# Kernel tuning notes

Measured on AMD Instinct MI355X. Metric: run time of the kernel, lower is better.

Reference implementation:

```python
import jax, jax.numpy as jnp
import numpy as np

N = 524288      # points per view
S = 256         # superpoint segments
SEG = N // S    # points per segment (2048 >= 30 -> no small segments)
C = 96          # backbone_out_channels
K = 30          # samples per segment (matching_max_pair//S = 32 >= 30 -> capped at 30)
NEG = 30        # negatives sampled per anchor row
T_SUP = 0.5     # SupConLoss temperature
EPS = 1e-7


def setup_inputs() -> dict:
    key = jax.random.key(0)
    ks = jax.random.split(key, 4)
    view1_feat = jax.random.normal(ks[0], (N, C), jnp.float32)
    view2_feat = jax.random.normal(ks[1], (N, C), jnp.float32)
    region = (jnp.arange(N, dtype=jnp.int32) // SEG).astype(jnp.int32)
    # evenly spaced K sample indices inside each contiguous segment
    off = jnp.linspace(0.0, SEG - 1, K).astype(jnp.int32)
    idx_samples = (jnp.arange(S, dtype=jnp.int32)[:, None] * SEG + off[None, :]).reshape(-1)
    bg_mask = (jnp.arange(S) % 4) == 0  # some background superpoints
    gq_w = jax.random.normal(ks[2], (C, C), jnp.float32) * 0.02
    gk_w = jax.random.normal(ks[3], (C, C), jnp.float32) * 0.02
    z = jnp.zeros((C,), jnp.float32)
    o = jnp.ones((C,), jnp.float32)
    return dict(view1_feat=view1_feat, view2_feat=view2_feat,
                gq_w=gq_w, gq_b=z, gq_gamma=o, gq_beta=z,
                gk_w=gk_w, gk_b=z, gk_gamma=o, gk_beta=z,
                view1_region=region, view2_region=region,
                idx_samples=idx_samples, bg_mask=bg_mask)


def _head(x, w, b, gamma, beta):
    # Linear -> BatchNorm1d (batch stats, training mode) -> ReLU
    y = x @ w.T + b
    mu = y.mean(axis=0)
    var = jnp.var(y, axis=0)
    y = (y - mu) * jax.lax.rsqrt(var + 1e-5) * gamma + beta
    return jax.nn.relu(y)


def _segment_mean(x, seg, n):
    s = jax.ops.segment_sum(x, seg, num_segments=n)
    cnt = jax.ops.segment_sum(jnp.ones((x.shape[0], 1), x.dtype), seg, num_segments=n)
    return s / jnp.maximum(cnt, 1.0)


def _l2norm(x):
    return x / (jnp.linalg.norm(x, axis=1, keepdims=True) + EPS)


def _supcon(sim, pos, neg):
    # SupConLoss(temperature=0.5, scale_by_temperature=False, is_positive_in_denom=True)
    logits = sim / T_SUP
    denom_mask = pos | neg
    neg_inf = jnp.finfo(logits.dtype).min
    lse = jax.scipy.special.logsumexp(jnp.where(denom_mask, logits, neg_inf), axis=1)
    log_prob = logits - lse[:, None]
    row = jnp.sum(jnp.where(pos, log_prob, 0.0), axis=1) / jnp.sum(pos, axis=1).astype(logits.dtype)
    return -jnp.mean(row)


def reference(view1_feat, view2_feat, gq_w, gq_b, gq_gamma, gq_beta,
              gk_w, gk_b, gk_gamma, gk_beta,
              view1_region, view2_region, idx_samples, bg_mask):
    Sk = S * K
    rows = jnp.arange(S)[:, None]

    # ---- Lcon: raw-feature superpoint anchors vs sampled points ----
    anchor = _l2norm(_segment_mean(view2_feat, view2_region, S))          # [S, C]
    samples = _l2norm(view1_feat[idx_samples])                            # [S*K, C]
    sim = anchor @ samples.T                                              # [S, S*K]

    col_seg = jnp.arange(Sk) // K
    pos1 = rows == col_seg[None, :]                                       # block-diagonal positives

    # 30 evenly spaced negatives among the Sk-K non-positive columns per row
    M = Sk - K
    p = jnp.linspace(0.0, M - 1, NEG).astype(jnp.int32)                   # [NEG]
    actual = jnp.where(p[None, :] < rows * K, p[None, :], p[None, :] + K) # skip own block
    neg1 = jnp.zeros((S, Sk), bool).at[jnp.broadcast_to(rows, (S, NEG)), actual].set(True)
    Lcon = _supcon(sim, pos1, neg1)

    # ---- Lcon_2: projected (g_q / g_k head) features, top-k positives, background-split negatives ----
    v2g = _head(view2_feat, gq_w, gq_b, gq_gamma, gq_beta)
    v1g = _head(view1_feat, gk_w, gk_b, gk_gamma, gk_beta)
    anchor2 = _l2norm(_segment_mean(v2g, view2_region, S))
    samples2 = _l2norm(v1g[idx_samples])
    sim2 = anchor2 @ samples2.T                                           # [S, S*K]

    _, tk = jax.lax.top_k(sim2, K)
    pos2 = jnp.zeros((S, Sk), bool).at[jnp.broadcast_to(rows, (S, K)), tk].set(True)

    bg_col = jnp.repeat(bg_mask, K)                                       # [S*K]
    neg2 = jnp.where(bg_mask[:, None], ~bg_col[None, :], bg_col[None, :]) & (~pos1)
    Lcon2 = _supcon(sim2, pos2, neg2)

    return Lcon + Lcon2


if __name__ == '__main__':
    out = reference(**setup_inputs())
    print(out)
```

## Files before the change

kernel.cpp:

```cpp
#include <hip/hip_runtime.h>
#include <math.h>

#define SK 7680
#define NPTS 524288

#define WS_GQ_PART  0
#define WS_GK_PART  6144
#define WS_GQ_SCALE 12288
#define WS_GQ_SHIFT 12384
#define WS_GK_SCALE 12480
#define WS_GK_SHIFT 12576
#define WS_SEGX2    21888
#define WS_SEGG2    46464
#define WS_ANCHOR1  71040
#define WS_ANCHOR2  95616
#define WS_SAMPT    120192
#define WS_SAMP2T   857472
#define WS_SROW     1594752
#define WS_ZERO_CNT 71040

typedef __attribute__((ext_vector_type(8))) short bf16x8;
typedef __attribute__((ext_vector_type(4))) float f32x4;

__device__ __forceinline__ bf16x8 pack8(float4 a, float4 b){
  union { unsigned u[4]; bf16x8 v; } r;
  asm("v_cvt_pk_bf16_f32 %0, %1, %2" : "=v"(r.u[0]) : "v"(a.x), "v"(a.y));
  asm("v_cvt_pk_bf16_f32 %0, %1, %2" : "=v"(r.u[1]) : "v"(a.z), "v"(a.w));
  asm("v_cvt_pk_bf16_f32 %0, %1, %2" : "=v"(r.u[2]) : "v"(b.x), "v"(b.y));
  asm("v_cvt_pk_bf16_f32 %0, %1, %2" : "=v"(r.u[3]) : "v"(b.z), "v"(b.w));
  return r.v;
}
__device__ __forceinline__ float4 ld4(const float* p){
  return *reinterpret_cast<const float4*>(p);
}

#define DS_ISSUE(r0,r1,r2,base,o0,o1,o2)                            \
  asm volatile("ds_read_b128 %0, %3 offset:" #o0 "\n\t"             \
               "ds_read_b128 %1, %3 offset:" #o1 "\n\t"             \
               "ds_read_b128 %2, %3 offset:" #o2                    \
               : "=v"(r0), "=v"(r1), "=v"(r2) : "v"(base));
#define DS_WAIT(n)                                                  \
  asm volatile("s_waitcnt lgkmcnt(" #n ")" ::: "memory");           \
  __builtin_amdgcn_sched_barrier(0);

#define MFMA3(acc, wx0, wx1, wx2)                                   \
  acc=__builtin_amdgcn_mfma_f32_16x16x32_bf16(a0,wx0,acc,0,0,0);    \
  acc=__builtin_amdgcn_mfma_f32_16x16x32_bf16(a1,wx1,acc,0,0,0);    \
  acc=__builtin_amdgcn_mfma_f32_16x16x32_bf16(a2,wx2,acc,0,0,0);

__device__ __forceinline__ void stage_wfrag(const float* __restrict__ W, float* wlds, int w, int l){
  if (w < 3){
    const int g = l >> 4, lr = l & 15;
    #pragma unroll
    for (int ot=0; ot<6; ++ot){
      const float* wr = W + (ot*16+lr)*96 + w*32 + g*8;
      bf16x8 f = pack8(ld4(wr), ld4(wr+4));
      *reinterpret_cast<bf16x8*>(wlds + ((w*6+ot)*64 + l)*4) = f;
    }
  }
}

__global__ __launch_bounds__(256) void stats_both(
    const float* __restrict__ V1, const float* __restrict__ V2,
    const float* __restrict__ Wk, const float* __restrict__ Wq,
    float* __restrict__ gpartK, float* __restrict__ gpartQ,
    float* __restrict__ gseg)
{
  __shared__ __align__(16) float wlds[4608];
  __shared__ float red[192];
  __shared__ float rsg[96];
  const int tid = threadIdx.x;
  const int l = tid & 63, w = tid >> 6;
  const int g = l >> 4, lr = l & 15;
  const int bid = blockIdx.x;
  const bool isv2 = (bid & 1);
  const int sub = bid >> 1;
  const float* X = isv2 ? V2 : V1;
  const float* W = isv2 ? Wq : Wk;

  stage_wfrag(W, wlds, w, l);
  if (tid < 192) red[tid]=0.f;
  if (isv2 && tid < 96) rsg[tid]=0.f;
  __syncthreads();

  const unsigned wbase = (unsigned)(uintptr_t)wlds + (unsigned)(l*16);

  float sY[6], sY2[6];
  #pragma unroll
  for (int ot=0; ot<6; ++ot){ sY[ot]=0.f; sY2[ot]=0.f; }
  float rs[24];
  #pragma unroll
  for (int t=0; t<24; ++t) rs[t]=0.f;

  const long base_row = (long)sub*256 + w*16 + lr;
  const float* xr0 = X + base_row*96 + g*8;

  float4 c0=ld4(xr0), c1=ld4(xr0+4), c2=ld4(xr0+32), c3=ld4(xr0+36), c4=ld4(xr0+64), c5=ld4(xr0+68);

#define STATS_OT(ot, wx0, wx1, wx2) {                               \
    f32x4 acc={0.f,0.f,0.f,0.f};                                    \
    MFMA3(acc, wx0, wx1, wx2)                                       \
    sY[ot]+=acc[0]+acc[1]+acc[2]+acc[3];                            \
    sY2[ot]=fmaf(acc[0],acc[0],fmaf(acc[1],acc[1],                  \
            fmaf(acc[2],acc[2],fmaf(acc[3],acc[3],sY2[ot])))); }

  #pragma unroll 1
  for (int it=0; it<4; ++it){
    float4 n0,n1,n2,n3,n4,n5;
    if (it<3){
      const float* xn = xr0 + (it+1)*6144;
      n0=ld4(xn); n1=ld4(xn+4); n2=ld4(xn+32); n3=ld4(xn+36); n4=ld4(xn+64); n5=ld4(xn+68);
    }
    if (isv2){
      rs[0]+=c0.x; rs[1]+=c0.y; rs[2]+=c0.z; rs[3]+=c0.w;
      rs[4]+=c1.x; rs[5]+=c1.y; rs[6]+=c1.z; rs[7]+=c1.w;
      rs[8]+=c2.x; rs[9]+=c2.y; rs[10]+=c2.z; rs[11]+=c2.w;
      rs[12]+=c3.x; rs[13]+=c3.y; rs[14]+=c3.z; rs[15]+=c3.w;
      rs[16]+=c4.x; rs[17]+=c4.y; rs[18]+=c4.z; rs[19]+=c4.w;
      rs[20]+=c5.x; rs[21]+=c5.y; rs[22]+=c5.z; rs[23]+=c5.w;
    }
    bf16x8 a0 = pack8(c0,c1), a1 = pack8(c2,c3), a2 = pack8(c4,c5);
    bf16x8 wA0,wA1,wA2, wB0,wB1,wB2;
    DS_ISSUE(wA0,wA1,wA2, wbase, 0,6144,12288)
    DS_ISSUE(wB0,wB1,wB2, wbase, 1024,7168,13312)
    DS_WAIT(3) STATS_OT(0, wA0,wA1,wA2)
    DS_ISSUE(wA0,wA1,wA2, wbase, 2048,8192,14336)
    DS_WAIT(3) STATS_OT(1, wB0,wB1,wB2)
    DS_ISSUE(wB0,wB1,wB2, wbase, 3072,9216,15360)
    DS_WAIT(3) STATS_OT(2, wA0,wA1,wA2)
    DS_ISSUE(wA0,wA1,wA2, wbase, 4096,10240,16384)
    DS_WAIT(3) STATS_OT(3, wB0,wB1,wB2)
    DS_ISSUE(wB0,wB1,wB2, wbase, 5120,11264,17408)
    DS_WAIT(3) STATS_OT(4, wA0,wA1,wA2)
    DS_WAIT(0) STATS_OT(5, wB0,wB1,wB2)
    if (it<3){ c0=n0; c1=n1; c2=n2; c3=n3; c4=n4; c5=n5; }
  }
#undef STATS_OT

  #pragma unroll
  for (int ot=0; ot<6; ++ot){
    float s = sY[ot], s2 = sY2[ot];
    s  += __shfl_xor(s,16);  s  += __shfl_xor(s,32);
    s2 += __shfl_xor(s2,16); s2 += __shfl_xor(s2,32);
    if (g==0){
      atomicAdd(&red[ot*16+lr], s);
      atomicAdd(&red[96+ot*16+lr], s2);
    }
  }
  if (isv2){
    #pragma unroll
    for (int t=0; t<24; ++t){
      float s = rs[t];
      s += __shfl_xor(s,1); s += __shfl_xor(s,2);
      s += __shfl_xor(s,4); s += __shfl_xor(s,8);
      if (lr==0){
        int kt = t>>3, j = t&7;
        atomicAdd(&rsg[kt*32 + g*8 + j], s);
      }
    }
  }
  __syncthreads();
  if (tid<96){
    float* dst = (isv2 ? gpartQ : gpartK) + (sub & 31)*192;
    atomicAdd(dst+tid,    red[tid]);
    atomicAdd(dst+96+tid, red[96+tid]);
    if (isv2) atomicAdd(gseg + (sub>>3)*96 + tid, rsg[tid]);
  }
}

__global__ __launch_bounds__(256) void head_apply_mfma(
    const float* __restrict__ X, const float* __restrict__ W,
    const float* __restrict__ scale, const float* __restrict__ shift,
    float* __restrict__ gseg)
{
  __shared__ __align__(16) float wlds[4608];
  __shared__ float red[96];
  const int tid = threadIdx.x;
  const int l = tid & 63, w = tid >> 6;
  const int g = l >> 4, lr = l & 15;

  stage_wfrag(W, wlds, w, l);
  if (tid < 96) red[tid]=0.f;
  __syncthreads();

  const unsigned wbase = (unsigned)(uintptr_t)wlds + (unsigned)(l*16);

  float sc[6], sh[6], zs[6];
  #pragma unroll
  for (int ot=0; ot<6; ++ot){
    sc[ot]=scale[ot*16+lr]; sh[ot]=shift[ot*16+lr]; zs[ot]=0.f;
  }

  const long base_row = (long)blockIdx.x*256 + w*16 + lr;
  const float* xr0 = X + base_row*96 + g*8;

  float4 c0=ld4(xr0), c1=ld4(xr0+4), c2=ld4(xr0+32), c3=ld4(xr0+36), c4=ld4(xr0+64), c5=ld4(xr0+68);

#define ZS_OT(ot, wx0, wx1, wx2) {                                  \
    f32x4 acc={0.f,0.f,0.f,0.f};                                    \
    MFMA3(acc, wx0, wx1, wx2)                                       \
    zs[ot]+=fmaxf(fmaf(acc[0],sc[ot],sh[ot]),0.f)                   \
           +fmaxf(fmaf(acc[1],sc[ot],sh[ot]),0.f)                   \
           +fmaxf(fmaf(acc[2],sc[ot],sh[ot]),0.f)                   \
           +fmaxf(fmaf(acc[3],sc[ot],sh[ot]),0.f); }

  #pragma unroll 1
  for (int it=0; it<4; ++it){
    float4 n0,n1,n2,n3,n4,n5;
    if (it<3){
      const float* xn = xr0 + (it+1)*6144;
      n0=ld4(xn); n1=ld4(xn+4); n2=ld4(xn+32); n3=ld4(xn+36); n4=ld4(xn+64); n5=ld4(xn+68);
    }
    bf16x8 a0 = pack8(c0,c1), a1 = pack8(c2,c3), a2 = pack8(c4,c5);
    bf16x8 wA0,wA1,wA2, wB0,wB1,wB2;
    DS_ISSUE(wA0,wA1,wA2, wbase, 0,6144,12288)
    DS_ISSUE(wB0,wB1,wB2, wbase, 1024,7168,13312)
    DS_WAIT(3) ZS_OT(0, wA0,wA1,wA2)
    DS_ISSUE(wA0,wA1,wA2, wbase, 2048,8192,14336)
    DS_WAIT(3) ZS_OT(1, wB0,wB1,wB2)
    DS_ISSUE(wB0,wB1,wB2, wbase, 3072,9216,15360)
    DS_WAIT(3) ZS_OT(2, wA0,wA1,wA2)
    DS_ISSUE(wA0,wA1,wA2, wbase, 4096,10240,16384)
    DS_WAIT(3) ZS_OT(3, wB0,wB1,wB2)
    DS_ISSUE(wB0,wB1,wB2, wbase, 5120,11264,17408)
    DS_WAIT(3) ZS_OT(4, wA0,wA1,wA2)
    DS_WAIT(0) ZS_OT(5, wB0,wB1,wB2)
    if (it<3){ c0=n0; c1=n1; c2=n2; c3=n3; c4=n4; c5=n5; }
  }
#undef ZS_OT

  #pragma unroll
  for (int ot=0; ot<6; ++ot){
    float s = zs[ot];
    s += __shfl_xor(s,16); s += __shfl_xor(s,32);
    if (g==0) atomicAdd(&red[ot*16+lr], s);
  }
  __syncthreads();
  if (tid<96) atomicAdd(gseg + (blockIdx.x>>3)*96 + tid, red[tid]);
}

__global__ void bn_params_kernel(const float* __restrict__ gq_gamma, const float* __restrict__ gq_beta,
                                 const float* __restrict__ gk_gamma, const float* __restrict__ gk_beta,
                                 float* __restrict__ ws)
{
  const int t = threadIdx.x;
  const float invN = 1.0f/(float)NPTS;
  if (t < 96){
    float s=0.f, s2=0.f;
    #pragma unroll 4
    for (int p=0;p<32;p++){
      s  += ws[WS_GQ_PART + p*192 + t];
      s2 += ws[WS_GQ_PART + p*192 + 96 + t];
    }
    float mu  = s*invN;
    float var = s2*invN - mu*mu;
    float sc  = gq_gamma[t]*rsqrtf(var + 1e-5f);
    ws[WS_GQ_SCALE+t] = sc;
    ws[WS_GQ_SHIFT+t] = gq_beta[t] - mu*sc;
  } else if (t < 192){
    int c = t-96;
    float s=0.f, s2=0.f;
    #pragma unroll 4
    for (int p=0;p<32;p++){
      s  += ws[WS_GK_PART + p*192 + c];
      s2 += ws[WS_GK_PART + p*192 + 96 + c];
    }
    float mu  = s*invN;
    float var = s2*invN - mu*mu;
    float sc  = gk_gamma[c]*rsqrtf(var + 1e-5f);
    ws[WS_GK_SCALE+c] = sc;
    ws[WS_GK_SHIFT+c] = gk_beta[c] - mu*sc;
  }
}

__global__ __launch_bounds__(128) void anchor2x_kernel(
    const float* __restrict__ seg1, float* __restrict__ dst1,
    const float* __restrict__ seg2, float* __restrict__ dst2)
{
  __shared__ float red[128];
  const int t = threadIdx.x, s = blockIdx.x & 255;
  const float* segsum = (blockIdx.x < 256) ? seg1 : seg2;
  float* dst          = (blockIdx.x < 256) ? dst1 : dst2;
  float m = 0.f;
  if (t<96) m = segsum[s*96+t] * (1.0f/2048.0f);
  red[t] = m*m;
  __syncthreads();
  for (int off=64; off>0; off>>=1){
    if (t<off) red[t]+=red[t+off];
    __syncthreads();
  }
  float inv = 1.0f/(sqrtf(red[0]) + 1e-7f);
  if (t<96) dst[s*96+t] = m*inv;
}

__device__ __forceinline__ void fma_row(float4& acc, const float4 x,
    const float4 w0, const float4 w1, const float4 w2, const float4 w3){
  acc.x = fmaf(x.x,w0.x, fmaf(x.y,w1.x, fmaf(x.z,w2.x, fmaf(x.w,w3.x, acc.x))));
  acc.y = fmaf(x.x,w0.y, fmaf(x.y,w1.y, fmaf(x.z,w2.y, fmaf(x.w,w3.y, acc.y))));
  acc.z = fmaf(x.x,w0.z, fmaf(x.y,w1.z, fmaf(x.z,w2.z, fmaf(x.w,w3.z, acc.z))));
  acc.w = fmaf(x.x,w0.w, fmaf(x.y,w1.w, fmaf(x.z,w2.w, fmaf(x.w,w3.w, acc.w))));
}
__device__ __forceinline__ void load_W(const float* __restrict__ W, float* Ws, int tid){
  #pragma unroll
  for (int i=0;i<12;i++){
    int f = i*768 + tid*4;
    int oc = f/96, k = f%96;
    float4 w4 = *reinterpret_cast<const float4*>(W + f);
    Ws[(k+0)*100+oc]=w4.x; Ws[(k+1)*100+oc]=w4.y;
    Ws[(k+2)*100+oc]=w4.z; Ws[(k+3)*100+oc]=w4.w;
  }
}
__device__ __forceinline__ void gemm_tile(const float* Xs, const float* Ws,
    int ocg, int rowg, int r0, float4 acc[4]){
  const float4* Xs4 = reinterpret_cast<const float4*>(Xs);
  const float4* Ws4 = reinterpret_cast<const float4*>(Ws);
  acc[0]=acc[1]=acc[2]=acc[3]=make_float4(0.f,0.f,0.f,0.f);
  #pragma unroll 4
  for (int k4=0;k4<24;k4++){
    float4 w0 = Ws4[(k4*4+0)*25 + ocg];
    float4 w1 = Ws4[(k4*4+1)*25 + ocg];
    float4 w2 = Ws4[(k4*4+2)*25 + ocg];
    float4 w3 = Ws4[(k4*4+3)*25 + ocg];
    #pragma unroll
    for (int jj=0;jj<4;jj++){
      float4 xv = Xs4[(r0+jj)*25 + (k4 ^ rowg)];
      fma_row(acc[jj], xv, w0, w1, w2, w3);
    }
  }
}

__global__ __launch_bounds__(192) void samples_kernel(
    const float* __restrict__ V1, const float* __restrict__ W,
    const float* __restrict__ scale, const float* __restrict__ shift,
    const int* __restrict__ idxs,
    float* __restrict__ sampT, float* __restrict__ samp2T)
{
  __shared__ __align__(16) float Ws[9600];
  __shared__ __align__(16) float Xs[3200];
  __shared__ __align__(16) float Gs[3200];
  __shared__ float invr[32], invh[32];
  const int tid = threadIdx.x;
  const int ocg = tid % 24, rowg = tid / 24;
  const int oc0 = ocg*4,  r0  = rowg*4;
  load_W(W, Ws, tid);
  const int base = blockIdx.x * 32;
  #pragma unroll
  for (int i=0;i<4;i++){
    int f = i*768 + tid*4;
    int row = f/96, col = f%96;
    int g = idxs[base+row];
    float4 v = *reinterpret_cast<const float4*>(V1 + g*96 + col);
    *reinterpret_cast<float4*>(Xs + row*100 + (col ^ ((row>>2)<<2))) = v;
  }
  __syncthreads();
  if (tid<32){
    float s=0.f;
    #pragma unroll
    for (int k=0;k<96;k++){ float v=Xs[tid*100+(k^((tid>>2)<<2))]; s=fmaf(v,v,s); }
    invr[tid]=1.0f/(sqrtf(s)+1e-7f);
  }
  __syncthreads();
  {
    int rr=tid&31, kg=tid>>5;
    float inv=invr[rr];
    #pragma unroll
    for (int kk=0;kk<16;kk++){
      int k=kg*16+kk;
      sampT[(long)(base+rr)*96 + k] = Xs[rr*100 + (k ^ ((rr>>2)<<2))]*inv;
    }
  }
  float4 acc[4];
  gemm_tile(Xs, Ws, ocg, rowg, r0, acc);
  float4 sc = make_float4(scale[oc0],scale[oc0+1],scale[oc0+2],scale[oc0+3]);
  float4 sh = make_float4(shift[oc0],shift[oc0+1],shift[oc0+2],shift[oc0+3]);
  #pragma unroll
  for (int jj=0;jj<4;jj++){
    int rr=r0+jj;
    float4 g;
    g.x=fmaxf(fmaf(acc[jj].x,sc.x,sh.x),0.f);
    g.y=fmaxf(fmaf(acc[jj].y,sc.y,sh.y),0.f);
    g.z=fmaxf(fmaf(acc[jj].z,sc.z,sh.z),0.f);
    g.w=fmaxf(fmaf(acc[jj].w,sc.w,sh.w),0.f);
    *reinterpret_cast<float4*>(Gs + rr*100 + (oc0 ^ ((rr>>2)<<2))) = g;
  }
  __syncthreads();
  if (tid<32){
    float s=0.f;
    #pragma unroll
    for (int k=0;k<96;k++){ float v=Gs[tid*100+(k^((tid>>2)<<2))]; s=fmaf(v,v,s); }
    invh[tid]=1.0f/(sqrtf(s)+1e-7f);
  }
  __syncthreads();
  {
    int rr=tid&31, kg=tid>>5;
    float inv=invh[rr];
    #pragma unroll
    for (int kk=0;kk<16;kk++){
      int k=kg*16+kk;
      samp2T[(long)(base+rr)*96 + k] = Gs[rr*100 + (k ^ ((rr>>2)<<2))]*inv;
    }
  }
}

__global__ __launch_bounds__(256) void sim2_mfma(
    const float* __restrict__ anchor2, const float* __restrict__ samp2,
    float* __restrict__ srowG)
{
  const int tid = threadIdx.x;
  const int l = tid & 63, w = tid >> 6;
  const int g = l >> 4, lr = l & 15;
  const int rowbase = blockIdx.y * 16;
  const int colbase = blockIdx.x * 256 + w * 64;

  bf16x8 af[3];
  const float* ar = anchor2 + (rowbase + lr)*96 + g*8;
  #pragma unroll
  for (int kt=0; kt<3; ++kt)
    af[kt] = pack8(ld4(ar + kt*32), ld4(ar + kt*32 + 4));

  #pragma unroll
  for (int sub=0; sub<4; ++sub){
    const float* br = samp2 + (long)(colbase + sub*16 + lr)*96 + g*8;
    float4 b00 = ld4(br);    float4 b01 = ld4(br+4);
    float4 b10 = ld4(br+32); float4 b11 = ld4(br+36);
    float4 b20 = ld4(br+64); float4 b21 = ld4(br+68);
    f32x4 acc = {0.f,0.f,0.f,0.f};
    acc = __builtin_amdgcn_mfma_f32_16x16x32_bf16(af[0], pack8(b00,b01), acc, 0,0,0);
    acc = __builtin_amdgcn_mfma_f32_16x16x32_bf16(af[1], pack8(b10,b11), acc, 0,0,0);
    acc = __builtin_amdgcn_mfma_f32_16x16x32_bf16(af[2], pack8(b20,b21), acc, 0,0,0);
    const int col  = colbase + sub*16 + lr;
    const int row0 = rowbase + g*4;
    #pragma unroll
    for (int i=0;i<4;i++)
      srowG[(long)(row0+i)*SK + col] = acc[i];
  }
}

__global__ __launch_bounds__(256) void lcon12_kernel(
    const float* __restrict__ anchor1, const float* __restrict__ sampT,
    const float* __restrict__ srowG, const int* __restrict__ bg,
    float* __restrict__ out)
{
  const int tid = threadIdx.x;
  if (blockIdx.x >= 256){
    __shared__ float a[96];
    const int r = blockIdx.x - 256;
    if (tid < 64){
      for (int i=tid;i<96;i+=64) a[i]=anchor1[r*96+i];
      int c = 0;
      if (tid<30) c = r*30+tid;
      else if (tid<60){
        int j = tid-30;
        int p = (int)((double)j * 7649.0 / 29.0);
        c = (p < r*30) ? p : p+30;
      }
      float s=0.f;
      if (tid<60){
        const float* sr = sampT + (long)c*96;
        #pragma unroll
        for (int k4=0;k4<24;k4++){
          float4 v = *reinterpret_cast<const float4*>(sr + k4*4);
          s = fmaf(a[k4*4+0],v.x, fmaf(a[k4*4+1],v.y,
              fmaf(a[k4*4+2],v.z, fmaf(a[k4*4+3],v.w, s))));
        }
      }
      float logit = 2.0f*s;
      float se = (tid<60) ? expf(logit) : 0.f;
      float sp = (tid<30) ? logit : 0.f;
      #pragma unroll
      for (int off=32; off; off>>=1){ se += __shfl_xor(se,off); sp += __shfl_xor(sp,off); }
      if (tid==0){
        float row = sp*(1.0f/30.0f) - logf(se);
        atomicAdd(out, -row*(1.0f/256.0f));
      }
    }
    return;
  }
  __shared__ float wvv[4];
  __shared__ int   wcc[4];
  __shared__ int   winc_s;
  __shared__ int   sel[30];
  const int r = blockIdx.x;
  const int lane = tid & 63, wid = tid >> 6;
  const float* __restrict__ rowp = srowG + (long)r*SK;
  float val[30];
  #pragma unroll
  for (int j=0;j<30;j++) val[j] = rowp[(j<<8) + tid];
  unsigned mask=0; float possum=0.f;
  for (int it=0; it<30; ++it){
    float bv = -3.0e38f; int bc = 1<<30;
    #pragma unroll
    for (int j=0;j<30;j++){
      if (!((mask>>j)&1u)){
        float v = val[j]; int c = tid + (j<<8);
        if (v > bv || (v == bv && c < bc)){ bv=v; bc=c; }
      }
    }
    #pragma unroll
    for (int off=32; off; off>>=1){
      float ov = __shfl_xor(bv, off); int ocx = __shfl_xor(bc, off);
      if (ov > bv || (ov == bv && ocx < bc)){ bv=ov; bc=ocx; }
    }
    if (lane==0){ wvv[wid]=bv; wcc[wid]=bc; }
    __syncthreads();
    if (tid==0){
      float v=wvv[0]; int c=wcc[0];
      #pragma unroll
      for (int w2=1;w2<4;w2++){
        if (wvv[w2]>v || (wvv[w2]==v && wcc[w2]<c)){ v=wvv[w2]; c=wcc[w2]; }
      }
      winc_s=c; sel[it]=c; possum += v;
    }
    __syncthreads();
    int c = winc_s;
    if ((c & 255) == tid) mask |= 1u << (c >> 8);
  }
  const int bgr = bg[r];
  float se=0.f;
  #pragma unroll
  for (int j=0;j<30;j++){
    int c = tid + (j<<8);
    int seg = c/30;
    int bgc = bg[seg];
    bool nf = ((bgr!=0) ? (bgc==0) : (bgc!=0)) && (seg != r);
    if (nf) se += expf(2.0f*val[j]);
  }
  #pragma unroll
  for (int off=32; off; off>>=1) se += __shfl_xor(se, off);
  if (lane==0) wvv[wid]=se;
  __syncthreads();
  float ex=0.f;
  if (tid<30){
    int c = sel[tid]; int seg=c/30; int bgc=bg[seg];
    bool nf = ((bgr!=0) ? (bgc==0) : (bgc!=0)) && (seg != r);
    if (!nf) ex = expf(2.0f*rowp[c]);
  }
  if (wid==0){
    #pragma unroll
    for (int off=32; off; off>>=1) ex += __shfl_xor(ex, off);
  }
  if (tid==0){
    float lse = logf(wvv[0]+wvv[1]+wvv[2]+wvv[3] + ex);
    float row = possum*(2.0f/30.0f) - lse;
    atomicAdd(out, -row*(1.0f/256.0f));
  }
}

extern "C" void kernel_launch(void* const* d_in, const int* in_sizes, int n_in,
                              void* d_out, int out_size, void* d_ws, size_t ws_size,
                              hipStream_t stream) {
  (void)in_sizes; (void)n_in; (void)out_size; (void)ws_size;
  const float* v1       = (const float*)d_in[0];
  const float* v2       = (const float*)d_in[1];
  const float* gq_w     = (const float*)d_in[2];
  const float* gq_gamma = (const float*)d_in[4];
  const float* gq_beta  = (const float*)d_in[5];
  const float* gk_w     = (const float*)d_in[6];
  const float* gk_gamma = (const float*)d_in[8];
  const float* gk_beta  = (const float*)d_in[9];
  const int*   idxs     = (const int*)d_in[12];
  const int*   bg       = (const int*)d_in[13];
  float* ws  = (float*)d_ws;
  float* out = (float*)d_out;

  hipMemsetAsync(ws, 0, (size_t)WS_ZERO_CNT*sizeof(float), stream);
  hipMemsetAsync(out, 0, sizeof(float), stream);

  stats_both<<<4096,256,0,stream>>>(v1, v2, gk_w, gq_w,
                                    ws+WS_GK_PART, ws+WS_GQ_PART, ws+WS_SEGX2);
  bn_params_kernel<<<1,192,0,stream>>>(gq_gamma, gq_beta, gk_gamma, gk_beta, ws);
  samples_kernel<<<240,192,0,stream>>>(v1, gk_w, ws+WS_GK_SCALE, ws+WS_GK_SHIFT, idxs,
                                       ws+WS_SAMPT, ws+WS_SAMP2T);
  head_apply_mfma<<<2048,256,0,stream>>>(v2, gq_w, ws+WS_GQ_SCALE, ws+WS_GQ_SHIFT, ws+WS_SEGG2);
  anchor2x_kernel<<<512,128,0,stream>>>(ws+WS_SEGX2, ws+WS_ANCHOR1, ws+WS_SEGG2, ws+WS_ANCHOR2);
  sim2_mfma<<<dim3(30,16),256,0,stream>>>(ws+WS_ANCHOR2, ws+WS_SAMP2T, ws+WS_SROW);
  lcon12_kernel<<<512,256,0,stream>>>(ws+WS_ANCHOR1, ws+WS_SAMPT, ws+WS_SROW, bg, out);
}
```

Measured before the change: 254.4 us.

## Stage input tiles via async global-to-LDS loads and keep weights in registers

Both MFMA head kernels now stream 32-row tiles of the input through a double-buffered, XOR-swizzled LDS buffer filled by global_load_lds, replacing direct per-lane vector loads. Weight fragments are held in registers, with each wave covering half the output channels, so the per-iteration LDS weight reads are gone. The raw view2 segment sum moves from stats_both into head_apply_mfma, which reads the same LDS tile. Each block now runs 8 iterations with two barriers per iteration, adding synchronization overhead and leaving correctness dependent on the hand-written vmcnt waits.

```diff
diff --git a/kernel.cpp b/kernel.cpp
--- a/kernel.cpp
+++ b/kernel.cpp
@@ -22,6 +22,13 @@
 typedef __attribute__((ext_vector_type(8))) short bf16x8;
 typedef __attribute__((ext_vector_type(4))) float f32x4;
 
+#define AS1 __attribute__((address_space(1)))
+#define AS3 __attribute__((address_space(3)))
+
+__device__ __forceinline__ void gl16(const float* g, char* l){
+  __builtin_amdgcn_global_load_lds((const AS1 unsigned*)g, (AS3 unsigned*)l, 16, 0, 0);
+}
+
 __device__ __forceinline__ bf16x8 pack8(float4 a, float4 b){
   union { unsigned u[4]; bf16x8 v; } r;
   asm("v_cvt_pk_bf16_f32 %0, %1, %2" : "=v"(r.u[0]) : "v"(a.x), "v"(a.y));
@@ -30,213 +37,246 @@
   asm("v_cvt_pk_bf16_f32 %0, %1, %2" : "=v"(r.u[3]) : "v"(b.z), "v"(b.w));
   return r.v;
 }
+__device__ __forceinline__ bf16x8 pack8v(f32x4 a, f32x4 b){
+  union { unsigned u[4]; bf16x8 v; } r;
+  asm("v_cvt_pk_bf16_f32 %0, %1, %2" : "=v"(r.u[0]) : "v"(a[0]), "v"(a[1]));
+  asm("v_cvt_pk_bf16_f32 %0, %1, %2" : "=v"(r.u[1]) : "v"(a[2]), "v"(a[3]));
+  asm("v_cvt_pk_bf16_f32 %0, %1, %2" : "=v"(r.u[2]) : "v"(b[0]), "v"(b[1]));
+  asm("v_cvt_pk_bf16_f32 %0, %1, %2" : "=v"(r.u[3]) : "v"(b[2]), "v"(b[3]));
+  return r.v;
+}
 __device__ __forceinline__ float4 ld4(const float* p){
   return *reinterpret_cast<const float4*>(p);
 }
 
-#define DS_ISSUE(r0,r1,r2,base,o0,o1,o2)                            \
-  asm volatile("ds_read_b128 %0, %3 offset:" #o0 "\n\t"             \
-               "ds_read_b128 %1, %3 offset:" #o1 "\n\t"             \
-               "ds_read_b128 %2, %3 offset:" #o2                    \
-               : "=v"(r0), "=v"(r1), "=v"(r2) : "v"(base));
-#define DS_WAIT(n)                                                  \
-  asm volatile("s_waitcnt lgkmcnt(" #n ")" ::: "memory");           \
-  __builtin_amdgcn_sched_barrier(0);
-
-#define MFMA3(acc, wx0, wx1, wx2)                                   \
-  acc=__builtin_amdgcn_mfma_f32_16x16x32_bf16(a0,wx0,acc,0,0,0);    \
-  acc=__builtin_amdgcn_mfma_f32_16x16x32_bf16(a1,wx1,acc,0,0,0);    \
-  acc=__builtin_amdgcn_mfma_f32_16x16x32_bf16(a2,wx2,acc,0,0,0);
-
-__device__ __forceinline__ void stage_wfrag(const float* __restrict__ W, float* wlds, int w, int l){
-  if (w < 3){
-    const int g = l >> 4, lr = l & 15;
-    #pragma unroll
-    for (int ot=0; ot<6; ++ot){
-      const float* wr = W + (ot*16+lr)*96 + w*32 + g*8;
-      bf16x8 f = pack8(ld4(wr), ld4(wr+4));
-      *reinterpret_cast<bf16x8*>(wlds + ((w*6+ot)*64 + l)*4) = f;
-    }
+__device__ __forceinline__ void build_wf(const float* __restrict__ W, bf16x8 wf[3][3],
+                                         int oh, int lr, int g){
+  #pragma unroll
+  for (int i=0;i<3;i++){
+    const float* wr = W + (unsigned)((oh*3+i)*16+lr)*96 + g*8;
+    #pragma unroll
+    for (int kt=0;kt<3;kt++)
+      wf[i][kt] = pack8(ld4(wr + kt*32), ld4(wr + kt*32 + 4));
   }
 }
 
 __global__ __launch_bounds__(256) void stats_both(
     const float* __restrict__ V1, const float* __restrict__ V2,
     const float* __restrict__ Wk, const float* __restrict__ Wq,
-    float* __restrict__ gpartK, float* __restrict__ gpartQ,
-    float* __restrict__ gseg)
+    float* __restrict__ gpartK, float* __restrict__ gpartQ)
 {
-  __shared__ __align__(16) float wlds[4608];
-  __shared__ float red[192];
+  __shared__ __align__(16) float xtile[2][3072];
+  __shared__ float red[96];
+  const int tid = threadIdx.x;
+  const int l = tid & 63, w = tid >> 6;
+  const int g = l >> 4, lr = l & 15;
+  const int rg = w & 1, oh = w >> 1;
+  const int R = rg*16 + lr;
+
+  const bool isv2 = (blockIdx.x & 1);
+  const int  sub  = blockIdx.x >> 1;
+  const float* X = isv2 ? V2 : V1;
+  const float* W = isv2 ? Wq : Wk;
+
+  bf16x8 wf[3][3];
+  build_wf(W, wf, oh, lr, g);
+  if (tid < 96) red[tid]=0.f;
+
+  int so[3];
+  #pragma unroll
+  for (int i=0;i<3;i++){
+    int s = i*256 + tid;
+    int r = s/24, cp = s%24;
+    int c = (cp & ~7) | ((cp & 7) ^ (r & 7));
+    so[i] = r*96 + c*4;
+  }
+  const float* base = X + (long)sub*24576;
+  char* lbase_c = (char*)&xtile[0][0] + w*1024;
+
+  unsigned lb = (unsigned)(uintptr_t)&xtile[0][0];
+  unsigned addrA = lb + R*384 + (unsigned)((( 2*g   ) ^ (R&7))*16);
+  unsigned addrB = lb + R*384 + (unsigned)((((2*g)|1) ^ (R&7))*16);
+
+#define STAGE(t, buf) {                                   \
+    const float* tb = base + (t)*3072;                    \
+    char* ld = lbase_c + (buf)*12288;                     \
+    gl16(tb + so[0], ld);                                 \
+    gl16(tb + so[1], ld + 4096);                          \
+    gl16(tb + so[2], ld + 8192); }
+
+  STAGE(0,0)
+  STAGE(1,1)
+
+  float sY[3]={0.f,0.f,0.f}, sY2[3]={0.f,0.f,0.f};
+
+  #pragma unroll 1
+  for (int it=0; it<8; ++it){
+    if (it<7){ asm volatile("s_waitcnt vmcnt(3)" ::: "memory"); }
+    else     { asm volatile("s_waitcnt vmcnt(0)" ::: "memory"); }
+    __builtin_amdgcn_s_barrier();
+    f32x4 xA0,xA1,xA2,xB0,xB1,xB2;
+    asm volatile(
+      "ds_read_b128 %0, %6\n\t"
+      "ds_read_b128 %1, %6 offset:128\n\t"
+      "ds_read_b128 %2, %6 offset:256\n\t"
+      "ds_read_b128 %3, %7\n\t"
+      "ds_read_b128 %4, %7 offset:128\n\t"
+      "ds_read_b128 %5, %7 offset:256\n\t"
+      "s_waitcnt lgkmcnt(0)"
+      : "=&v"(xA0),"=&v"(xA1),"=&v"(xA2),"=&v"(xB0),"=&v"(xB1),"=&v"(xB2)
+      : "v"(addrA), "v"(addrB) : "memory");
+    __builtin_amdgcn_sched_barrier(0);
+    __builtin_amdgcn_s_barrier();
+    if (it<6) STAGE(it+2, it&1)
+    bf16x8 a0 = pack8v(xA0,xB0), a1 = pack8v(xA1,xB1), a2 = pack8v(xA2,xB2);
+    #pragma unroll
+    for (int i=0;i<3;i++){
+      f32x4 acc = {0.f,0.f,0.f,0.f};
+      acc = __builtin_amdgcn_mfma_f32_16x16x32_bf16(a0, wf[i][0], acc, 0,0,0);
+      acc = __builtin_amdgcn_mfma_f32_16x16x32_bf16(a1, wf[i][1], acc, 0,0,0);
+      acc = __builtin_amdgcn_mfma_f32_16x16x32_bf16(a2, wf[i][2], acc, 0,0,0);
+      sY[i]  += acc[0]+acc[1]+acc[2]+acc[3];
+      sY2[i]  = fmaf(acc[0],acc[0],fmaf(acc[1],acc[1],
+                fmaf(acc[2],acc[2],fmaf(acc[3],acc[3],sY2[i]))));
+    }
+    addrA ^= 12288u; addrB ^= 12288u;
+  }
+#undef STAGE
+
+  __shared__ float red2[96];
+  if (tid < 96) red2[tid]=0.f;
+  __syncthreads();
+  #pragma unroll
+  for (int i=0;i<3;i++){
+    float s = sY[i], s2 = sY2[i];
+    s  += __shfl_xor(s,16);  s  += __shfl_xor(s,32);
+    s2 += __shfl_xor(s2,16); s2 += __shfl_xor(s2,32);
+    if (g==0){
+      atomicAdd(&red[(oh*3+i)*16+lr],  s);
+      atomicAdd(&red2[(oh*3+i)*16+lr], s2);
+    }
+  }
+  __syncthreads();
+  if (tid<96){
+    float* dst = (isv2 ? gpartQ : gpartK) + (sub & 31)*192;
+    atomicAdd(dst+tid,    red[tid]);
+    atomicAdd(dst+96+tid, red2[tid]);
+  }
+}
+
+__global__ __launch_bounds__(256) void head_apply_mfma(
+    const float* __restrict__ X, const float* __restrict__ W,
+    const float* __restrict__ scale, const float* __restrict__ shift,
+    float* __restrict__ gsegRaw, float* __restrict__ gsegBN)
+{
+  __shared__ __align__(16) float xtile[2][3072];
+  __shared__ float red[96];
   __shared__ float rsg[96];
   const int tid = threadIdx.x;
   const int l = tid & 63, w = tid >> 6;
   const int g = l >> 4, lr = l & 15;
-  const int bid = blockIdx.x;
-  const bool isv2 = (bid & 1);
-  const int sub = bid >> 1;
-  const float* X = isv2 ? V2 : V1;
-  const float* W = isv2 ? Wq : Wk;
-
-  stage_wfrag(W, wlds, w, l);
-  if (tid < 192) red[tid]=0.f;
-  if (isv2 && tid < 96) rsg[tid]=0.f;
-  __syncthreads();
-
-  const unsigned wbase = (unsigned)(uintptr_t)wlds + (unsigned)(l*16);
-
-  float sY[6], sY2[6];
-  #pragma unroll
-  for (int ot=0; ot<6; ++ot){ sY[ot]=0.f; sY2[ot]=0.f; }
-  float rs[24];
-  #pragma unroll
-  for (int t=0; t<24; ++t) rs[t]=0.f;
-
-  const long base_row = (long)sub*256 + w*16 + lr;
-  const float* xr0 = X + base_row*96 + g*8;
-
-  float4 c0=ld4(xr0), c1=ld4(xr0+4), c2=ld4(xr0+32), c3=ld4(xr0+36), c4=ld4(xr0+64), c5=ld4(xr0+68);
-
-#define STATS_OT(ot, wx0, wx1, wx2) {                               \
-    f32x4 acc={0.f,0.f,0.f,0.f};                                    \
-    MFMA3(acc, wx0, wx1, wx2)                                       \
-    sY[ot]+=acc[0]+acc[1]+acc[2]+acc[3];                            \
-    sY2[ot]=fmaf(acc[0],acc[0],fmaf(acc[1],acc[1],                  \
-            fmaf(acc[2],acc[2],fmaf(acc[3],acc[3],sY2[ot])))); }
+  const int rg = w & 1, oh = w >> 1;
+  const int R = rg*16 + lr;
+
+  bf16x8 wf[3][3];
+  build_wf(W, wf, oh, lr, g);
+  if (tid < 96){ red[tid]=0.f; rsg[tid]=0.f; }
+
+  float sc[3], sh[3];
+  #pragma unroll
+  for (int i=0;i<3;i++){
+    sc[i]=scale[(oh*3+i)*16+lr]; sh[i]=shift[(oh*3+i)*16+lr];
+  }
+
+  int so[3], ck[3];
+  #pragma unroll
+  for (int i=0;i<3;i++){
+    int s = i*256 + tid;
+    int r = s/24, cp = s%24;
+    int c = (cp & ~7) | ((cp & 7) ^ (r & 7));
+    so[i] = r*96 + c*4;
+    ck[i] = c;
+  }
+  const float* base = X + (long)blockIdx.x*24576;
+  char* lbase_c = (char*)&xtile[0][0] + w*1024;
+
+  unsigned lb = (unsigned)(uintptr_t)&xtile[0][0];
+  unsigned addrA = lb + R*384 + (unsigned)((( 2*g   ) ^ (R&7))*16);
+  unsigned addrB = lb + R*384 + (unsigned)((((2*g)|1) ^ (R&7))*16);
+  unsigned addrC = lb + tid*16;
+
+#define STAGE(t, buf) {                                   \
+    const float* tb = base + (t)*3072;                    \
+    char* ld = lbase_c + (buf)*12288;                     \
+    gl16(tb + so[0], ld);                                 \
+    gl16(tb + so[1], ld + 4096);                          \
+    gl16(tb + so[2], ld + 8192); }
+
+  STAGE(0,0)
+  STAGE(1,1)
+
+  float zs[3]={0.f,0.f,0.f};
+  f32x4 cs0={0.f,0.f,0.f,0.f}, cs1={0.f,0.f,0.f,0.f}, cs2={0.f,0.f,0.f,0.f};
 
   #pragma unroll 1
-  for (int it=0; it<4; ++it){
-    float4 n0,n1,n2,n3,n4,n5;
-    if (it<3){
-      const float* xn = xr0 + (it+1)*6144;
-      n0=ld4(xn); n1=ld4(xn+4); n2=ld4(xn+32); n3=ld4(xn+36); n4=ld4(xn+64); n5=ld4(xn+68);
-    }
-    if (isv2){
-      rs[0]+=c0.x; rs[1]+=c0.y; rs[2]+=c0.z; rs[3]+=c0.w;
-      rs[4]+=c1.x; rs[5]+=c1.y; rs[6]+=c1.z; rs[7]+=c1.w;
-      rs[8]+=c2.x; rs[9]+=c2.y; rs[10]+=c2.z; rs[11]+=c2.w;
-      rs[12]+=c3.x; rs[13]+=c3.y; rs[14]+=c3.z; rs[15]+=c3.w;
-      rs[16]+=c4.x; rs[17]+=c4.y; rs[18]+=c4.z; rs[19]+=c4.w;
-      rs[20]+=c5.x; rs[21]+=c5.y; rs[22]+=c5.z; rs[23]+=c5.w;
-    }
-    bf16x8 a0 = pack8(c0,c1), a1 = pack8(c2,c3), a2 = pack8(c4,c5);
-    bf16x8 wA0,wA1,wA2, wB0,wB1,wB2;
-    DS_ISSUE(wA0,wA1,wA2, wbase, 0,6144,12288)
-    DS_ISSUE(wB0,wB1,wB2, wbase, 1024,7168,13312)
-    DS_WAIT(3) STATS_OT(0, wA0,wA1,wA2)
-    DS_ISSUE(wA0,wA1,wA2, wbase, 2048,8192,14336)
-    DS_WAIT(3) STATS_OT(1, wB0,wB1,wB2)
-    DS_ISSUE(wB0,wB1,wB2, wbase, 3072,9216,15360)
-    DS_WAIT(3) STATS_OT(2, wA0,wA1,wA2)
-    DS_ISSUE(wA0,wA1,wA2, wbase, 4096,10240,16384)
-    DS_WAIT(3) STATS_OT(3, wB0,wB1,wB2)
-    DS_ISSUE(wB0,wB1,wB2, wbase, 5120,11264,17408)
-    DS_WAIT(3) STATS_OT(4, wA0,wA1,wA2)
-    DS_WAIT(0) STATS_OT(5, wB0,wB1,wB2)
-    if (it<3){ c0=n0; c1=n1; c2=n2; c3=n3; c4=n4; c5=n5; }
-  }
-#undef STATS_OT
-
-  #pragma unroll
-  for (int ot=0; ot<6; ++ot){
-    float s = sY[ot], s2 = sY2[ot];
-    s  += __shfl_xor(s,16);  s  += __shfl_xor(s,32);
-    s2 += __shfl_xor(s2,16); s2 += __shfl_xor(s2,32);
-    if (g==0){
-      atomicAdd(&red[ot*16+lr], s);
-      atomicAdd(&red[96+ot*16+lr], s2);
-    }
-  }
-  if (isv2){
-    #pragma unroll
-    for (int t=0; t<24; ++t){
-      float s = rs[t];
-      s += __shfl_xor(s,1); s += __shfl_xor(s,2);
-      s += __shfl_xor(s,4); s += __shfl_xor(s,8);
-      if (lr==0){
-        int kt = t>>3, j = t&7;
-        atomicAdd(&rsg[kt*32 + g*8 + j], s);
-      }
-    }
+  for (int it=0; it<8; ++it){
+    if (it<7){ asm volatile("s_waitcnt vmcnt(3)" ::: "memory"); }
+    else     { asm volatile("s_waitcnt vmcnt(0)" ::: "memory"); }
+    __builtin_amdgcn_s_barrier();
+    f32x4 xA0,xA1,xA2,xB0,xB1,xB2,xC0,xC1,xC2;
+    asm volatile(
+      "ds_read_b128 %0, %9\n\t"
+      "ds_read_b128 %1, %9 offset:128\n\t"
+      "ds_read_b128 %2, %9 offset:256\n\t"
+      "ds_read_b128 %3, %10\n\t"
+      "ds_read_b128 %4, %10 offset:128\n\t"
+      "ds_read_b128 %5, %10 offset:256\n\t"
+      "ds_read_b128 %6, %11\n\t"
+      "ds_read_b128 %7, %11 offset:4096\n\t"
+      "ds_read_b128 %8, %11 offset:8192\n\t"
+      "s_waitcnt lgkmcnt(0)"
+      : "=&v"(xA0),"=&v"(xA1),"=&v"(xA2),"=&v"(xB0),"=&v"(xB1),"=&v"(xB2),
+        "=&v"(xC0),"=&v"(xC1),"=&v"(xC2)
+      : "v"(addrA), "v"(addrB), "v"(addrC) : "memory");
+    __builtin_amdgcn_sched_barrier(0);
+    __builtin_amdgcn_s_barrier();
+    if (it<6) STAGE(it+2, it&1)
+    cs0[0]+=xC0[0]; cs0[1]+=xC0[1]; cs0[2]+=xC0[2]; cs0[3]+=xC0[3];
+    cs1[0]+=xC1[0]; cs1[1]+=xC1[1]; cs1[2]+=xC1[2]; cs1[3]+=xC1[3];
+    cs2[0]+=xC2[0]; cs2[1]+=xC2[1]; cs2[2]+=xC2[2]; cs2[3]+=xC2[3];
+    bf16x8 a0 = pack8v(xA0,xB0), a1 = pack8v(xA1,xB1), a2 = pack8v(xA2,xB2);
+    #pragma unroll
+    for (int i=0;i<3;i++){
+      f32x4 acc = {0.f,0.f,0.f,0.f};
+      acc = __builtin_amdgcn_mfma_f32_16x16x32_bf16(a0, wf[i][0], acc, 0,0,0);
+      acc = __builtin_amdgcn_mfma_f32_16x16x32_bf16(a1, wf[i][1], acc, 0,0,0);
+      acc = __builtin_amdgcn_mfma_f32_16x16x32_bf16(a2, wf[i][2], acc, 0,0,0);
+      zs[i] += fmaxf(fmaf(acc[0],sc[i],sh[i]),0.f)
+             + fmaxf(fmaf(acc[1],sc[i],sh[i]),0.f)
+             + fmaxf(fmaf(acc[2],sc[i],sh[i]),0.f)
+             + fmaxf(fmaf(acc[3],sc[i],sh[i]),0.f);
+    }
+    addrA ^= 12288u; addrB ^= 12288u; addrC ^= 12288u;
+  }
+#undef STAGE
+
+  #pragma unroll
+  for (int k=0;k<4;k++) atomicAdd(&rsg[ck[0]*4+k], cs0[k]);
+  #pragma unroll
+  for (int k=0;k<4;k++) atomicAdd(&rsg[ck[1]*4+k], cs1[k]);
+  #pragma unroll
+  for (int k=0;k<4;k++) atomicAdd(&rsg[ck[2]*4+k], cs2[k]);
+  #pragma unroll
+  for (int i=0;i<3;i++){
+    float s = zs[i];
+    s += __shfl_xor(s,16); s += __shfl_xor(s,32);
+    if (g==0) atomicAdd(&red[(oh*3+i)*16+lr], s);
   }
   __syncthreads();
   if (tid<96){
-    float* dst = (isv2 ? gpartQ : gpartK) + (sub & 31)*192;
-    atomicAdd(dst+tid,    red[tid]);
-    atomicAdd(dst+96+tid, red[96+tid]);
-    if (isv2) atomicAdd(gseg + (sub>>3)*96 + tid, rsg[tid]);
-  }
-}
-
-__global__ __launch_bounds__(256) void head_apply_mfma(
-    const float* __restrict__ X, const float* __restrict__ W,
-    const float* __restrict__ scale, const float* __restrict__ shift,
-    float* __restrict__ gseg)
-{
-  __shared__ __align__(16) float wlds[4608];
-  __shared__ float red[96];
-  const int tid = threadIdx.x;
-  const int l = tid & 63, w = tid >> 6;
-  const int g = l >> 4, lr = l & 15;
-
-  stage_wfrag(W, wlds, w, l);
-  if (tid < 96) red[tid]=0.f;
-  __syncthreads();
-
-  const unsigned wbase = (unsigned)(uintptr_t)wlds + (unsigned)(l*16);
-
-  float sc[6], sh[6], zs[6];
-  #pragma unroll
-  for (int ot=0; ot<6; ++ot){
-    sc[ot]=scale[ot*16+lr]; sh[ot]=shift[ot*16+lr]; zs[ot]=0.f;
-  }
-
-  const long base_row = (long)blockIdx.x*256 + w*16 + lr;
-  const float* xr0 = X + base_row*96 + g*8;
-
-  float4 c0=ld4(xr0), c1=ld4(xr0+4), c2=ld4(xr0+32), c3=ld4(xr0+36), c4=ld4(xr0+64), c5=ld4(xr0+68);
-
-#define ZS_OT(ot, wx0, wx1, wx2) {                                  \
-    f32x4 acc={0.f,0.f,0.f,0.f};                                    \
-    MFMA3(acc, wx0, wx1, wx2)                                       \
-    zs[ot]+=fmaxf(fmaf(acc[0],sc[ot],sh[ot]),0.f)                   \
-           +fmaxf(fmaf(acc[1],sc[ot],sh[ot]),0.f)                   \
-           +fmaxf(fmaf(acc[2],sc[ot],sh[ot]),0.f)                   \
-           +fmaxf(fmaf(acc[3],sc[ot],sh[ot]),0.f); }
-
-  #pragma unroll 1
-  for (int it=0; it<4; ++it){
-    float4 n0,n1,n2,n3,n4,n5;
-    if (it<3){
-      const float* xn = xr0 + (it+1)*6144;
-      n0=ld4(xn); n1=ld4(xn+4); n2=ld4(xn+32); n3=ld4(xn+36); n4=ld4(xn+64); n5=ld4(xn+68);
-    }
-    bf16x8 a0 = pack8(c0,c1), a1 = pack8(c2,c3), a2 = pack8(c4,c5);
-    bf16x8 wA0,wA1,wA2, wB0,wB1,wB2;
-    DS_ISSUE(wA0,wA1,wA2, wbase, 0,6144,12288)
-    DS_ISSUE(wB0,wB1,wB2, wbase, 1024,7168,13312)
-    DS_WAIT(3) ZS_OT(0, wA0,wA1,wA2)
-    DS_ISSUE(wA0,wA1,wA2, wbase, 2048,8192,14336)
-    DS_WAIT(3) ZS_OT(1, wB0,wB1,wB2)
-    DS_ISSUE(wB0,wB1,wB2, wbase, 3072,9216,15360)
-    DS_WAIT(3) ZS_OT(2, wA0,wA1,wA2)
-    DS_ISSUE(wA0,wA1,wA2, wbase, 4096,10240,16384)
-    DS_WAIT(3) ZS_OT(3, wB0,wB1,wB2)
-    DS_ISSUE(wB0,wB1,wB2, wbase, 5120,11264,17408)
-    DS_WAIT(3) ZS_OT(4, wA0,wA1,wA2)
-    DS_WAIT(0) ZS_OT(5, wB0,wB1,wB2)
-    if (it<3){ c0=n0; c1=n1; c2=n2; c3=n3; c4=n4; c5=n5; }
-  }
-#undef ZS_OT
-
-  #pragma unroll
-  for (int ot=0; ot<6; ++ot){
-    float s = zs[ot];
-    s += __shfl_xor(s,16); s += __shfl_xor(s,32);
-    if (g==0) atomicAdd(&red[ot*16+lr], s);
-  }
-  __syncthreads();
-  if (tid<96) atomicAdd(gseg + (blockIdx.x>>3)*96 + tid, red[tid]);
+    atomicAdd(gsegRaw + (blockIdx.x>>3)*96 + tid, rsg[tid]);
+    atomicAdd(gsegBN  + (blockIdx.x>>3)*96 + tid, red[tid]);
+  }
 }
 
 __global__ void bn_params_kernel(const float* __restrict__ gq_gamma, const float* __restrict__ gq_beta,
@@ -566,12 +606,12 @@
   hipMemsetAsync(ws, 0, (size_t)WS_ZERO_CNT*sizeof(float), stream);
   hipMemsetAsync(out, 0, sizeof(float), stream);
 
-  stats_both<<<4096,256,0,stream>>>(v1, v2, gk_w, gq_w,
-                                    ws+WS_GK_PART, ws+WS_GQ_PART, ws+WS_SEGX2);
+  stats_both<<<4096,256,0,stream>>>(v1, v2, gk_w, gq_w, ws+WS_GK_PART, ws+WS_GQ_PART);
   bn_params_kernel<<<1,192,0,stream>>>(gq_gamma, gq_beta, gk_gamma, gk_beta, ws);
   samples_kernel<<<240,192,0,stream>>>(v1, gk_w, ws+WS_GK_SCALE, ws+WS_GK_SHIFT, idxs,
                                        ws+WS_SAMPT, ws+WS_SAMP2T);
-  head_apply_mfma<<<2048,256,0,stream>>>(v2, gq_w, ws+WS_GQ_SCALE, ws+WS_GQ_SHIFT, ws+WS_SEGG2);
+  head_apply_mfma<<<2048,256,0,stream>>>(v2, gq_w, ws+WS_GQ_SCALE, ws+WS_GQ_SHIFT,
+                                         ws+WS_SEGX2, ws+WS_SEGG2);
   anchor2x_kernel<<<512,128,0,stream>>>(ws+WS_SEGX2, ws+WS_ANCHOR1, ws+WS_SEGG2, ws+WS_ANCHOR2);
   sim2_mfma<<<dim3(30,16),256,0,stream>>>(ws+WS_ANCHOR2, ws+WS_SAMP2T, ws+WS_SROW);
   lcon12_kernel<<<512,256,0,stream>>>(ws+WS_ANCHOR1, ws+WS_SAMPT, ws+WS_SROW, bg, out);
```

Measured after the change: 258.7 us. No clear change (+1.7%).
